# Optimization experiments

Measured on AMD Instinct MI355X. Metric: run time of the kernel, lower is better.

Reference implementation:

```python
import jax, jax.numpy as jnp
import numpy as np

B, S, D = 8, 2048, 512
H, LAT, OUT = 8, 64, 64


def setup_inputs() -> dict:
    key = jax.random.key(0)
    ks = jax.random.split(key, 5)
    return {
        "x": jax.random.normal(ks[0], (B, S, D), dtype=jnp.float32),
        "WQ": jax.random.normal(ks[1], (H, D, LAT), dtype=jnp.float32) * 0.05,
        "WK": jax.random.normal(ks[2], (H, D, LAT), dtype=jnp.float32) * 0.05,
        "WV": jax.random.normal(ks[3], (H, D, OUT), dtype=jnp.float32) * 0.05,
        "WO": jax.random.normal(ks[4], (H * OUT, OUT), dtype=jnp.float32) * 0.05,
    }


def reference(x, WQ, WK, WV, WO):
    # Per-head projections, vectorized over heads (faithful to the TF python loop).
    Q = jnp.einsum('bsd,hdk->bhsk', x, WQ)   # [B,H,S,LAT]
    K = jnp.einsum('bsd,hdk->bhsk', x, WK)   # [B,H,S,LAT]
    V = jnp.einsum('bsd,hdo->bhso', x, WV)   # [B,H,S,OUT]
    scale = jnp.asarray(1.0 / np.sqrt(LAT), dtype=x.dtype)
    A = jnp.einsum('bhqk,bhsk->bhqs', Q, K) * scale  # [B,H,S,S]
    A = jax.nn.softmax(A, axis=-1)
    O = jnp.einsum('bhqs,bhso->bhqo', A, V)  # [B,H,S,OUT]
    # concat heads along last axis (head 0 first, matching the TF loop order)
    O = jnp.transpose(O, (0, 2, 1, 3)).reshape(x.shape[0], x.shape[1], H * OUT)
    return O @ WO  # [B,S,OUT]
```

## Files before the change

kernel.cpp:

```cpp
#include <hip/hip_runtime.h>
#include <hip/hip_bf16.h>
#include <math.h>

static constexpr int Bn = 8, Sn = 2048, Dn = 512, Hn = 8, LATn = 64, OUTn = 64;

typedef short  bf16x8 __attribute__((ext_vector_type(8)));
typedef float  f32x4  __attribute__((ext_vector_type(4)));

__device__ __forceinline__ unsigned short f2bf(float f) {
    union { float f; unsigned int i; } v; v.f = f;
    unsigned int x = v.i;
    return (unsigned short)((x + 0x7FFFu + ((x >> 16) & 1u)) >> 16);
}
__device__ __forceinline__ unsigned int pack2bf(float a, float b) {
    unsigned int ua = __float_as_uint(a) + 0x8000u;
    unsigned int ub = __float_as_uint(b) + 0x8000u;
    return (ua >> 16) | (ub & 0xFFFF0000u);
}

#if __has_builtin(__builtin_amdgcn_exp2f)
#define EXP2(x) __builtin_amdgcn_exp2f(x)
#else
#define EXP2(x) exp2f(x)
#endif

__device__ __forceinline__ void gl_lds16(const void* g, void* l) {
    __builtin_amdgcn_global_load_lds(
        (const __attribute__((address_space(1))) unsigned int*)g,
        (__attribute__((address_space(3))) unsigned int*)l, 16, 0, 0);
}

__global__ __launch_bounds__(256) void wprep(
    const float* __restrict__ WQ, const float* __restrict__ WK,
    const float* __restrict__ WV, const float* __restrict__ WO,
    unsigned short* __restrict__ WT)
{
    __shared__ float tile[64][65];
    const int t  = threadIdx.x;
    const int d0 = blockIdx.x * 64;
    const int yy = blockIdx.y;

    const float* W; float scale = 1.0f; size_t dstbase;
    if (yy < 24) {
        int h = yy / 3, which = yy % 3;
        W = (which == 0) ? WQ : (which == 1) ? WK : WV;
        W += (size_t)h * Dn * 64;
        if (which == 0) scale = 0.125f * 1.44269504088896f;
        dstbase = ((size_t)h * 192 + which * 64) * Dn;
    } else {
        W = WO;
        dstbase = (size_t)8 * 192 * Dn;
    }

    for (int i = 0; i < 4; ++i) {
        int idx = i * 256 + t;
        int r = idx >> 4, c = (idx & 15) * 4;
        float4 u = *(const float4*)(W + (size_t)(d0 + r) * 64 + c);
        tile[r][c] = u.x; tile[r][c+1] = u.y; tile[r][c+2] = u.z; tile[r][c+3] = u.w;
    }
    __syncthreads();
    const int n = t & 63, dd = t >> 6;
    unsigned short pk[16];
    for (int i = 0; i < 16; ++i) pk[i] = f2bf(tile[dd*16 + i][n] * scale);
    size_t dst = dstbase + (size_t)n * Dn + d0 + dd * 16;
    *(bf16x8*)(WT + dst)     = *(bf16x8*)(pk);
    *(bf16x8*)(WT + dst + 8) = *(bf16x8*)(pk + 8);
}

__global__ __launch_bounds__(256) void qkv_mfma(
    const float* __restrict__ x, const unsigned short* __restrict__ WT,
    unsigned short* __restrict__ Qb, unsigned short* __restrict__ Kb,
    unsigned short* __restrict__ VT)
{
    __shared__ __align__(16) unsigned short lds[64*72 + 192*72];
    unsigned short* Xs = lds;
    unsigned short* Ws = lds + 64*72;
    unsigned short* L  = lds;

    const int t  = threadIdx.x;
    const int w  = t >> 6, ln = t & 63;
    const int nl = ln & 15, g = ln >> 4;
    const int bh = blockIdx.y, b = bh >> 3, h = bh & 7;
    const int s0 = blockIdx.x * 64;

    f32x4 acc[4][3];
    for (int m = 0; m < 4; ++m)
        for (int j = 0; j < 3; ++j) acc[m][j] = (f32x4){0.f, 0.f, 0.f, 0.f};

    for (int k0 = 0; k0 < Dn; k0 += 64) {
        __syncthreads();
        for (int i = 0; i < 2; ++i) {
            int idx = i * 256 + t;
            int r = idx >> 3, c = (idx & 7) * 8;
            const float* src = x + ((size_t)(b * Sn + s0 + r)) * Dn + k0 + c;
            float4 u0 = *(const float4*)(src);
            float4 u1 = *(const float4*)(src + 4);
            unsigned int pk[4] = { pack2bf(u0.x, u0.y), pack2bf(u0.z, u0.w),
                                   pack2bf(u1.x, u1.y), pack2bf(u1.z, u1.w) };
            *(bf16x8*)(Xs + r*72 + c) = *(bf16x8*)pk;
        }
        for (int i = 0; i < 6; ++i) {
            int idx = i * 256 + t;
            int r = idx >> 3, c = (idx & 7) * 8;
            *(bf16x8*)(Ws + r*72 + c) =
                *(const bf16x8*)(WT + ((size_t)h * 192 + r) * Dn + k0 + c);
        }
        __syncthreads();
        #pragma unroll
        for (int kc = 0; kc < 2; ++kc) {
            bf16x8 a[4], bb[3];
            for (int m = 0; m < 4; ++m)
                a[m]  = *(const bf16x8*)(Xs + (16*m + nl)*72 + 32*kc + 8*g);
            for (int j = 0; j < 3; ++j)
                bb[j] = *(const bf16x8*)(Ws + ((3*w + j)*16 + nl)*72 + 32*kc + 8*g);
            for (int m = 0; m < 4; ++m)
                for (int j = 0; j < 3; ++j)
                    acc[m][j] = __builtin_amdgcn_mfma_f32_16x16x32_bf16(
                                    a[m], bb[j], acc[m][j], 0, 0, 0);
        }
    }
    __syncthreads();
    for (int m = 0; m < 4; ++m)
        for (int j = 0; j < 3; ++j) {
            int n = 48*w + 16*j + nl;
            for (int r = 0; r < 4; ++r)
                L[(16*m + 4*g + r)*200 + n] = f2bf(acc[m][j][r]);
        }
    __syncthreads();
    for (int i = 0; i < 4; ++i) {
        int idx = i * 256 + t;
        int r = idx >> 4, c = (idx & 15) * 8;
        bf16x8 v = *(const bf16x8*)(L + r*200 + c);
        size_t o = ((size_t)bh * Sn + s0 + r) * 64;
        if (c < 64) *(bf16x8*)(Qb + o + c)      = v;
        else        *(bf16x8*)(Kb + o + c - 64) = v;
    }
    {
        int o = t & 63, cc = t >> 6;
        unsigned short pk[16];
        for (int i = 0; i < 16; ++i) {
            int srow = 32*(cc>>1) + 16*((i>>2)&1) + 8*(cc&1) + 4*((i>>3)&1) + (i&3);
            pk[i] = L[srow*200 + 128 + o];
        }
        size_t dst = ((size_t)bh * 64 + o) * Sn + s0 + 16*cc;
        *(bf16x8*)(VT + dst)     = *(bf16x8*)(pk);
        *(bf16x8*)(VT + dst + 8) = *(bf16x8*)(pk + 8);
    }
}

__global__ __launch_bounds__(256, 2) void flash_mfma(
    const unsigned short* __restrict__ Qb,
    const unsigned short* __restrict__ Kb,
    const unsigned short* __restrict__ VT,
    unsigned short* __restrict__ Ob)
{
    __shared__ __align__(16) unsigned short KV[2][2][4096];

    const int t  = threadIdx.x;
    const int w  = t >> 6, ln = t & 63;
    const int qh = ln & 15, g = (ln >> 4) & 3;
    const int bh = blockIdx.y, b = bh >> 3, h = bh & 7;
    const int q0 = blockIdx.x * 256;
    const int qw = q0 + 64 * w;

    bf16x8 bq[4][2];
    #pragma unroll
    for (int qs = 0; qs < 4; ++qs) {
        const unsigned short* qp =
            Qb + ((size_t)bh * Sn + qw + 16*qs + qh) * 64 + 8*g;
        bq[qs][0] = *(const bf16x8*)(qp);
        bq[qs][1] = *(const bf16x8*)(qp + 32);
    }

    const int r0a = t >> 3;
    const int csa = (t & 7) ^ (r0a & 7);
    const int r0b = 32 + (t >> 3);
    const int csb = (t & 7) ^ (r0b & 7);
    const unsigned short* kga = Kb + ((size_t)bh * Sn + r0a) * 64 + csa * 8;
    const unsigned short* kgb = Kb + ((size_t)bh * Sn + r0b) * 64 + csb * 8;
    const unsigned short* vga = VT + ((size_t)bh * 64 + r0a) * Sn + csa * 8;
    const unsigned short* vgb = VT + ((size_t)bh * 64 + r0b) * Sn + csb * 8;

    const int koff0 = qh*64 + (((g    ) ^ (qh & 7)) * 8);
    const int koff1 = qh*64 + (((4 + g) ^ (qh & 7)) * 8);

    f32x4 o_acc[4][4];
    #pragma unroll
    for (int qs = 0; qs < 4; ++qs)
        #pragma unroll
        for (int f = 0; f < 4; ++f) o_acc[qs][f] = (f32x4){0.f, 0.f, 0.f, 0.f};
    float l_run[4] = {0.f, 0.f, 0.f, 0.f};

    gl_lds16(kga, &KV[0][0][w * 512]);
    gl_lds16(kgb, &KV[0][0][2048 + w * 512]);
    gl_lds16(vga, &KV[0][1][w * 512]);
    gl_lds16(vgb, &KV[0][1][2048 + w * 512]);
    __syncthreads();

    int buf = 0;
    for (int kt = 0; kt < Sn / 64; ++kt) {
        if (kt < Sn / 64 - 1) {
            kga += 4096; kgb += 4096; vga += 64; vgb += 64;
            gl_lds16(kga, &KV[buf ^ 1][0][w * 512]);
            gl_lds16(kgb, &KV[buf ^ 1][0][2048 + w * 512]);
            gl_lds16(vga, &KV[buf ^ 1][1][w * 512]);
            gl_lds16(vgb, &KV[buf ^ 1][1][2048 + w * 512]);
        }
        const unsigned short* Kt = KV[buf][0];
        const unsigned short* Vt = KV[buf][1];

        f32x4 st[4][4];
        #pragma unroll
        for (int qs = 0; qs < 4; ++qs)
            #pragma unroll
            for (int f = 0; f < 4; ++f) st[qs][f] = (f32x4){0.f, 0.f, 0.f, 0.f};
        #pragma unroll
        for (int kc = 0; kc < 2; ++kc) {
            const int ko = kc ? koff1 : koff0;
            bf16x8 a0 = *(const bf16x8*)(Kt + ko);
            bf16x8 a1 = *(const bf16x8*)(Kt + ko + 1024);
            bf16x8 a2 = *(const bf16x8*)(Kt + ko + 2048);
            bf16x8 a3 = *(const bf16x8*)(Kt + ko + 3072);
            #pragma unroll
            for (int qs = 0; qs < 4; ++qs) {
                st[qs][0] = __builtin_amdgcn_mfma_f32_16x16x32_bf16(a0, bq[qs][kc], st[qs][0], 0, 0, 0);
                st[qs][1] = __builtin_amdgcn_mfma_f32_16x16x32_bf16(a1, bq[qs][kc], st[qs][1], 0, 0, 0);
                st[qs][2] = __builtin_amdgcn_mfma_f32_16x16x32_bf16(a2, bq[qs][kc], st[qs][2], 0, 0, 0);
                st[qs][3] = __builtin_amdgcn_mfma_f32_16x16x32_bf16(a3, bq[qs][kc], st[qs][3], 0, 0, 0);
            }
        }

        bf16x8 bp[4][2];
        #pragma unroll
        for (int qs = 0; qs < 4; ++qs) {
            float e0[4], e1[4], e2[4], e3[4];
            #pragma unroll
            for (int r = 0; r < 4; ++r) {
                e0[r] = EXP2(st[qs][0][r]);
                e1[r] = EXP2(st[qs][1][r]);
                e2[r] = EXP2(st[qs][2][r]);
                e3[r] = EXP2(st[qs][3][r]);
            }
            l_run[qs] += ((e0[0]+e0[1])+(e0[2]+e0[3])) + ((e1[0]+e1[1])+(e1[2]+e1[3]))
                       + ((e2[0]+e2[1])+(e2[2]+e2[3])) + ((e3[0]+e3[1])+(e3[2]+e3[3]));
            unsigned int p0[4] = { pack2bf(e0[0],e0[1]), pack2bf(e0[2],e0[3]),
                                   pack2bf(e1[0],e1[1]), pack2bf(e1[2],e1[3]) };
            unsigned int p1[4] = { pack2bf(e2[0],e2[1]), pack2bf(e2[2],e2[3]),
                                   pack2bf(e3[0],e3[1]), pack2bf(e3[2],e3[3]) };
            bp[qs][0] = *(bf16x8*)p0;
            bp[qs][1] = *(bf16x8*)p1;
        }

        #pragma unroll
        for (int kc = 0; kc < 2; ++kc) {
            const int ko = kc ? koff1 : koff0;
            bf16x8 v0 = *(const bf16x8*)(Vt + ko);
            bf16x8 v1 = *(const bf16x8*)(Vt + ko + 1024);
            bf16x8 v2 = *(const bf16x8*)(Vt + ko + 2048);
            bf16x8 v3 = *(const bf16x8*)(Vt + ko + 3072);
            #pragma unroll
            for (int qs = 0; qs < 4; ++qs) {
                o_acc[qs][0] = __builtin_amdgcn_mfma_f32_16x16x32_bf16(v0, bp[qs][kc], o_acc[qs][0], 0, 0, 0);
                o_acc[qs][1] = __builtin_amdgcn_mfma_f32_16x16x32_bf16(v1, bp[qs][kc], o_acc[qs][1], 0, 0, 0);
                o_acc[qs][2] = __builtin_amdgcn_mfma_f32_16x16x32_bf16(v2, bp[qs][kc], o_acc[qs][2], 0, 0, 0);
                o_acc[qs][3] = __builtin_amdgcn_mfma_f32_16x16x32_bf16(v3, bp[qs][kc], o_acc[qs][3], 0, 0, 0);
            }
        }

        __syncthreads();
        buf ^= 1;
    }

    #pragma unroll
    for (int qs = 0; qs < 4; ++qs) {
        l_run[qs] += __shfl_xor(l_run[qs], 16);
        l_run[qs] += __shfl_xor(l_run[qs], 32);
    }

    #pragma unroll
    for (int qs = 0; qs < 4; ++qs) {
        float inv_l = 1.f / l_run[qs];
        unsigned short* op = Ob
            + ((size_t)(b * Sn + q0 + 64*w + 16*qs + qh)) * 512 + h*64 + 4*g;
        #pragma unroll
        for (int f = 0; f < 4; ++f) {
            unsigned int lo = pack2bf(o_acc[qs][f][0] * inv_l, o_acc[qs][f][1] * inv_l);
            unsigned int hi = pack2bf(o_acc[qs][f][2] * inv_l, o_acc[qs][f][3] * inv_l);
            *(uint2*)(op + 16*f) = make_uint2(lo, hi);
        }
    }
}

__global__ __launch_bounds__(256) void out_mfma(
    const unsigned short* __restrict__ Ob, const unsigned short* __restrict__ WOT,
    float* __restrict__ out)
{
    __shared__ __align__(16) unsigned short As[64 * 72];
    __shared__ __align__(16) unsigned short Bs[64 * 72];

    const int t  = threadIdx.x;
    const int w  = t >> 6, ln = t & 63;
    const int qh = ln & 15, g = ln >> 4;
    const int bs0 = blockIdx.x * 64;

    f32x4 acc[4];
    for (int n = 0; n < 4; ++n) acc[n] = (f32x4){0.f, 0.f, 0.f, 0.f};

    for (int k0 = 0; k0 < 512; k0 += 64) {
        __syncthreads();
        for (int i = 0; i < 2; ++i) {
            int idx = i * 256 + t;
            int r = idx >> 3, c = (idx & 7) * 8;
            *(bf16x8*)(As + r*72 + c) =
                *(const bf16x8*)(Ob + ((size_t)(bs0 + r)) * 512 + k0 + c);
            *(bf16x8*)(Bs + r*72 + c) =
                *(const bf16x8*)(WOT + (size_t)r * Dn + k0 + c);
        }
        __syncthreads();
        #pragma unroll
        for (int kc = 0; kc < 2; ++kc) {
            bf16x8 a = *(const bf16x8*)(As + (16*w + qh)*72 + 32*kc + 8*g);
            #pragma unroll
            for (int n = 0; n < 4; ++n) {
                bf16x8 bb = *(const bf16x8*)(Bs + (16*n + qh)*72 + 32*kc + 8*g);
                acc[n] = __builtin_amdgcn_mfma_f32_16x16x32_bf16(a, bb, acc[n], 0, 0, 0);
            }
        }
    }
    for (int n = 0; n < 4; ++n)
        for (int r = 0; r < 4; ++r)
            out[((size_t)(bs0 + 16*w + 4*g + r)) * 64 + 16*n + qh] = acc[n][r];
}

extern "C" void kernel_launch(void* const* d_in, const int* in_sizes, int n_in,
                              void* d_out, int out_size, void* d_ws, size_t ws_size,
                              hipStream_t stream)
{
    const float* x  = (const float*)d_in[0];
    const float* WQ = (const float*)d_in[1];
    const float* WK = (const float*)d_in[2];
    const float* WV = (const float*)d_in[3];
    const float* WO = (const float*)d_in[4];
    float* out = (float*)d_out;

    const size_t NQ = (size_t)Bn * Hn * Sn * LATn;
    char* p = (char*)d_ws;
    unsigned short* Qb  = (unsigned short*)p;           p += NQ * 2;
    unsigned short* Kb  = (unsigned short*)p;           p += NQ * 2;
    unsigned short* VT  = (unsigned short*)p;           p += NQ * 2;
    unsigned short* WT  = (unsigned short*)p;           p += ((size_t)Hn*192*Dn + 64*Dn) * 2;
    unsigned short* Ob  = (unsigned short*)p;
    unsigned short* WOT = WT + (size_t)Hn * 192 * Dn;

    wprep     <<<dim3(8, 25),         256, 0, stream>>>(WQ, WK, WV, WO, WT);
    qkv_mfma  <<<dim3(Sn/64, Bn*Hn),  256, 0, stream>>>(x, WT, Qb, Kb, VT);
    flash_mfma<<<dim3(Sn/256, Bn*Hn), 256, 0, stream>>>(Qb, Kb, VT, Ob);
    out_mfma  <<<dim3(Bn*Sn/64),      256, 0, stream>>>(Ob, WOT, out);
}
```

Before: 207.1 us.

## Triple-buffer K/V tiles with vmcnt waits, add MFMA priority and hardware bf16 pack

The flash attention kernel moves from a double-buffered to a triple-buffered LDS ring for K/V tiles. It prefetches two tiles ahead and uses explicit vmcnt waits plus a single barrier per iteration in place of the trailing __syncthreads. MFMA sections are wrapped in s_setprio so one wave's matrix work can interleave with another's exp work, and the manual bf16 packing is replaced by the v_cvt_pk_bf16_f32 instruction. This raises LDS use per block, which may limit occupancy at 2 blocks/CU, and the pack now rounds differently.

After: 208.4 us. Within noise of the previous version (+0.6%).

```diff
diff --git a/kernel.cpp b/kernel.cpp
--- a/kernel.cpp
+++ b/kernel.cpp
@@ -16,6 +16,11 @@
     unsigned int ua = __float_as_uint(a) + 0x8000u;
     unsigned int ub = __float_as_uint(b) + 0x8000u;
     return (ua >> 16) | (ub & 0xFFFF0000u);
+}
+__device__ __forceinline__ unsigned int cvtpk(float a, float b) {
+    unsigned int r;
+    asm("v_cvt_pk_bf16_f32 %0, %1, %2" : "=v"(r) : "v"(a), "v"(b));
+    return r;
 }
 
 #if __has_builtin(__builtin_amdgcn_exp2f)
@@ -154,7 +159,7 @@
     const unsigned short* __restrict__ VT,
     unsigned short* __restrict__ Ob)
 {
-    __shared__ __align__(16) unsigned short KV[2][2][4096];
+    __shared__ __align__(16) unsigned short KV[3][2][4096];
 
     const int t  = threadIdx.x;
     const int w  = t >> 6, ln = t & 63;
@@ -191,20 +196,29 @@
         for (int f = 0; f < 4; ++f) o_acc[qs][f] = (f32x4){0.f, 0.f, 0.f, 0.f};
     float l_run[4] = {0.f, 0.f, 0.f, 0.f};
 
-    gl_lds16(kga, &KV[0][0][w * 512]);
-    gl_lds16(kgb, &KV[0][0][2048 + w * 512]);
-    gl_lds16(vga, &KV[0][1][w * 512]);
-    gl_lds16(vgb, &KV[0][1][2048 + w * 512]);
-    __syncthreads();
-
-    int buf = 0;
-    for (int kt = 0; kt < Sn / 64; ++kt) {
-        if (kt < Sn / 64 - 1) {
-            kga += 4096; kgb += 4096; vga += 64; vgb += 64;
-            gl_lds16(kga, &KV[buf ^ 1][0][w * 512]);
-            gl_lds16(kgb, &KV[buf ^ 1][0][2048 + w * 512]);
-            gl_lds16(vga, &KV[buf ^ 1][1][w * 512]);
-            gl_lds16(vgb, &KV[buf ^ 1][1][2048 + w * 512]);
+    gl_lds16(kga,        &KV[0][0][w * 512]);
+    gl_lds16(kgb,        &KV[0][0][2048 + w * 512]);
+    gl_lds16(vga,        &KV[0][1][w * 512]);
+    gl_lds16(vgb,        &KV[0][1][2048 + w * 512]);
+    gl_lds16(kga + 4096, &KV[1][0][w * 512]);
+    gl_lds16(kgb + 4096, &KV[1][0][2048 + w * 512]);
+    gl_lds16(vga + 64,   &KV[1][1][w * 512]);
+    gl_lds16(vgb + 64,   &KV[1][1][2048 + w * 512]);
+
+    constexpr int NT = Sn / 64;
+    int buf = 0, sbuf = 2;
+    for (int kt = 0; kt < NT; ++kt) {
+        if (kt < NT - 1) asm volatile("s_waitcnt vmcnt(4)" ::: "memory");
+        else             asm volatile("s_waitcnt vmcnt(0)" ::: "memory");
+        __builtin_amdgcn_s_barrier();
+
+        if (kt < NT - 2) {
+            const size_t ko = (size_t)(kt + 2) * 4096;
+            const int    vo = (kt + 2) * 64;
+            gl_lds16(kga + ko, &KV[sbuf][0][w * 512]);
+            gl_lds16(kgb + ko, &KV[sbuf][0][2048 + w * 512]);
+            gl_lds16(vga + vo, &KV[sbuf][1][w * 512]);
+            gl_lds16(vgb + vo, &KV[sbuf][1][2048 + w * 512]);
         }
         const unsigned short* Kt = KV[buf][0];
         const unsigned short* Vt = KV[buf][1];
@@ -214,6 +228,7 @@
         for (int qs = 0; qs < 4; ++qs)
             #pragma unroll
             for (int f = 0; f < 4; ++f) st[qs][f] = (f32x4){0.f, 0.f, 0.f, 0.f};
+        __builtin_amdgcn_s_setprio(1);
         #pragma unroll
         for (int kc = 0; kc < 2; ++kc) {
             const int ko = kc ? koff1 : koff0;
@@ -229,6 +244,7 @@
                 st[qs][3] = __builtin_amdgcn_mfma_f32_16x16x32_bf16(a3, bq[qs][kc], st[qs][3], 0, 0, 0);
             }
         }
+        __builtin_amdgcn_s_setprio(0);
 
         bf16x8 bp[4][2];
         #pragma unroll
@@ -243,14 +259,15 @@
             }
             l_run[qs] += ((e0[0]+e0[1])+(e0[2]+e0[3])) + ((e1[0]+e1[1])+(e1[2]+e1[3]))
                        + ((e2[0]+e2[1])+(e2[2]+e2[3])) + ((e3[0]+e3[1])+(e3[2]+e3[3]));
-            unsigned int p0[4] = { pack2bf(e0[0],e0[1]), pack2bf(e0[2],e0[3]),
-                                   pack2bf(e1[0],e1[1]), pack2bf(e1[2],e1[3]) };
-            unsigned int p1[4] = { pack2bf(e2[0],e2[1]), pack2bf(e2[2],e2[3]),
-                                   pack2bf(e3[0],e3[1]), pack2bf(e3[2],e3[3]) };
+            unsigned int p0[4] = { cvtpk(e0[0],e0[1]), cvtpk(e0[2],e0[3]),
+                                   cvtpk(e1[0],e1[1]), cvtpk(e1[2],e1[3]) };
+            unsigned int p1[4] = { cvtpk(e2[0],e2[1]), cvtpk(e2[2],e2[3]),
+                                   cvtpk(e3[0],e3[1]), cvtpk(e3[2],e3[3]) };
             bp[qs][0] = *(bf16x8*)p0;
             bp[qs][1] = *(bf16x8*)p1;
         }
 
+        __builtin_amdgcn_s_setprio(1);
         #pragma unroll
         for (int kc = 0; kc < 2; ++kc) {
             const int ko = kc ? koff1 : koff0;
@@ -266,9 +283,10 @@
                 o_acc[qs][3] = __builtin_amdgcn_mfma_f32_16x16x32_bf16(v3, bp[qs][kc], o_acc[qs][3], 0, 0, 0);
             }
         }
-
-        __syncthreads();
-        buf ^= 1;
+        __builtin_amdgcn_s_setprio(0);
+
+        buf  = (buf  == 2) ? 0 : buf  + 1;
+        sbuf = (sbuf == 2) ? 0 : sbuf + 1;
     }
 
     #pragma unroll
@@ -284,8 +302,8 @@
             + ((size_t)(b * Sn + q0 + 64*w + 16*qs + qh)) * 512 + h*64 + 4*g;
         #pragma unroll
         for (int f = 0; f < 4; ++f) {
-            unsigned int lo = pack2bf(o_acc[qs][f][0] * inv_l, o_acc[qs][f][1] * inv_l);
-            unsigned int hi = pack2bf(o_acc[qs][f][2] * inv_l, o_acc[qs][f][3] * inv_l);
+            unsigned int lo = cvtpk(o_acc[qs][f][0] * inv_l, o_acc[qs][f][1] * inv_l);
+            unsigned int hi = cvtpk(o_acc[qs][f][2] * inv_l, o_acc[qs][f][3] * inv_l);
             *(uint2*)(op + 16*f) = make_uint2(lo, hi);
         }
     }
```
